# Optimization experiments

Hardware: AMD Instinct MI355X
Metric: run time of the kernel (lower is better)

Reference implementation:

```python
import jax, jax.numpy as jnp
import numpy as np

B = 1024
HP_ORDER = 4
N_GRID = 72 * (8 ** HP_ORDER)  # 294912 rotations in the SO(3) healpix grid


def _random_rotmats(key, n):
    """Uniform random rotation matrices via normalized quaternions."""
    q = jax.random.normal(key, (n, 4), dtype=jnp.float32)
    q = q / jnp.linalg.norm(q, axis=-1, keepdims=True)
    w, x, y, z = q[:, 0], q[:, 1], q[:, 2], q[:, 3]
    R = jnp.stack([
        jnp.stack([1 - 2 * (y * y + z * z), 2 * (x * y - w * z), 2 * (x * z + w * y)], axis=-1),
        jnp.stack([2 * (x * y + w * z), 1 - 2 * (x * x + z * z), 2 * (y * z - w * x)], axis=-1),
        jnp.stack([2 * (x * z - w * y), 2 * (y * z + w * x), 1 - 2 * (x * x + y * y)], axis=-1),
    ], axis=-2)  # [n, 3, 3]
    return R


def setup_inputs() -> dict:
    key = jax.random.key(0)
    k1, k2 = jax.random.split(key)
    rotMat = _random_rotmats(k1, B)            # [B, 3, 3] query rotations
    output_rotmats = _random_rotmats(k2, N_GRID)  # [N, 3, 3] fixed grid (buffer)
    return {"rotMat": rotMat, "output_rotmats": output_rotmats}


def reference(rotMat, output_rotmats):
    # trace(A @ R_n^T) == sum_ij A_ij * R_n_ij  -> GEMM with K=9
    sim = jnp.einsum('bij,nij->bn', rotMat, output_rotmats)  # [B, N]
    idxs = jnp.argmax(sim, axis=1)                            # [B]
    dot_trace = jnp.max(sim, axis=1)                          # [B]
    nearest = output_rotmats[idxs]                            # [B, 3, 3]
    return dot_trace, nearest
```

## Files before the change

kernel.cpp:

```cpp
#include <hip/hip_runtime.h>

#define B_TOTAL 1024
#define NGRID   294912
#define NBLK    1024
#define CHUNK   (NGRID / NBLK)
#define NTHR    128
#define BPT     8


__global__ __launch_bounds__(256)
void so3_init_kernel(unsigned long long* __restrict__ ws) {
    int i = blockIdx.x * 256 + threadIdx.x;
    if (i < B_TOTAL) ws[i] = 0ull;
}

__global__ __launch_bounds__(NTHR, 3)
void so3_partial_kernel(const float* __restrict__ A,
                        const float* __restrict__ G,
                        unsigned long long* __restrict__ ws)
{
    __shared__ __align__(16) float sG[CHUNK * 12];

    const int t  = threadIdx.x;
    const int n0 = blockIdx.x * CHUNK;

    for (int i = t; i < CHUNK * 9; i += NTHR) {
        int row = i / 9, k = i - row * 9;
        sG[row * 12 + k] = G[(size_t)n0 * 9 + i];
    }

    float a[BPT][9];
    #pragma unroll
    for (int j = 0; j < BPT; ++j) {
        const float* ap = A + (size_t)(j * NTHR + t) * 9;
        #pragma unroll
        for (int k = 0; k < 9; ++k) a[j][k] = ap[k];
    }

    float best[BPT];
    int   bidx[BPT];
    #pragma unroll
    for (int j = 0; j < BPT; ++j) { best[j] = -1e30f; bidx[j] = 0; }

    __syncthreads();

    #pragma unroll 2
    for (int n = 0; n < CHUNK; ++n) {
        const float4* gv = (const float4*)(sG + n * 12);
        const float4 gA = gv[0], gB = gv[1];
        const float  g8 = sG[n * 12 + 8];
        const int vn = n0 + n;
        #pragma unroll
        for (int j = 0; j < BPT; ++j) {
            float d;
            d = a[j][0] * gA.x;
            d = fmaf(a[j][1], gA.y, d);
            d = fmaf(a[j][2], gA.z, d);
            d = fmaf(a[j][3], gA.w, d);
            d = fmaf(a[j][4], gB.x, d);
            d = fmaf(a[j][5], gB.y, d);
            d = fmaf(a[j][6], gB.z, d);
            d = fmaf(a[j][7], gB.w, d);
            d = fmaf(a[j][8], g8, d);
            if (d > best[j]) { best[j] = d; bidx[j] = vn; }
        }
    }

    #pragma unroll
    for (int j = 0; j < BPT; ++j) {
        unsigned u = __float_as_uint(best[j]);
        u = (u & 0x80000000u) ? ~u : (u | 0x80000000u);
        unsigned long long key =
            ((unsigned long long)u << 32) | (unsigned)(~bidx[j]);
        atomicMax(&ws[j * NTHR + t], key);
    }
}

__global__ __launch_bounds__(256)
void so3_final_kernel(const float* __restrict__ G,
                      const unsigned long long* __restrict__ ws,
                      float* __restrict__ out)
{
    int b = blockIdx.x * 256 + threadIdx.x;
    if (b >= B_TOTAL) return;
    unsigned long long key = ws[b];
    unsigned hi = (unsigned)(key >> 32);
    unsigned lo = (unsigned)key;
    unsigned bits = (hi & 0x80000000u) ? (hi ^ 0x80000000u) : ~hi;
    int idx = (int)(~lo);
    out[b] = __uint_as_float(bits);
    const float* g = G + (size_t)idx * 9;
    float* o = out + B_TOTAL + (size_t)b * 9;
    #pragma unroll
    for (int k = 0; k < 9; ++k) o[k] = g[k];
}

extern "C" void kernel_launch(void* const* d_in, const int* in_sizes, int n_in,
                              void* d_out, int out_size, void* d_ws, size_t ws_size,
                              hipStream_t stream) {
    const float* A = (const float*)d_in[0];
    const float* G = (const float*)d_in[1];
    float* out = (float*)d_out;
    unsigned long long* ws = (unsigned long long*)d_ws;

    hipLaunchKernelGGL(so3_init_kernel,    dim3(4),    dim3(256), 0, stream, ws);
    hipLaunchKernelGGL(so3_partial_kernel, dim3(NBLK), dim3(NTHR), 0, stream, A, G, ws);
    hipLaunchKernelGGL(so3_final_kernel,   dim3(4),    dim3(256), 0, stream, G, ws, out);
}
```

Measured before the change: 96.77 us.

## Use split-bf16 MFMA max pass with candidate filtering and exact fp32 rescoring

Replaces the scalar fp32 FMA scan with bf16 MFMA matrix products. A and G are packed into hi/lo bf16 pairs so that three-term products approximate fp32 accuracy. A first MFMA pass computes per-query maxima, and a second pass emits every (query, grid) pair within a margin of that max as a candidate. The candidates are then rescored exactly in fp32 for the argmax. This trades compute-bound FMA work for matrix-core throughput, but adds packing kernels, two full passes over the GEMM, atomics on a global candidate counter, and reliance on the margin and candidate cap being correct. The old scalar path is kept as a fallback when the workspace is too small.

```diff
diff --git a/kernel.cpp b/kernel.cpp
--- a/kernel.cpp
+++ b/kernel.cpp
@@ -2,97 +2,279 @@
 
 #define B_TOTAL 1024
 #define NGRID   294912
-#define NBLK    1024
-#define CHUNK   (NGRID / NBLK)
-#define NTHR    128
-#define BPT     8
-
+#define NTILES  (NGRID / 16)
+#define MARGIN  6e-4f
+#define CAP     (1u << 20)
+
+#define KEYS_OFF   0u
+#define WSMAX_OFF  8192u
+#define CNT_OFF    12288u
+#define CAND_OFF   16384u
+#define APACK_OFF  4210688u
+#define GPACK_OFF  4276224u
+#define WS_NEED    23150592u
+
+typedef __attribute__((ext_vector_type(8))) short short8v;
+typedef __attribute__((ext_vector_type(4))) float float4v;
+
+__device__ __forceinline__ unsigned short f2bf(float x) {
+    unsigned u = __float_as_uint(x);
+    unsigned r = ((u >> 16) & 1u) + 0x7FFFu;
+    return (unsigned short)((u + r) >> 16);
+}
+__device__ __forceinline__ float bf2f(unsigned short b) {
+    return __uint_as_float(((unsigned)b) << 16);
+}
+__device__ __forceinline__ unsigned ford(float f) {
+    unsigned u = __float_as_uint(f);
+    return (u & 0x80000000u) ? ~u : (u | 0x80000000u);
+}
+__device__ __forceinline__ float funord(unsigned u) {
+    return __uint_as_float((u & 0x80000000u) ? (u & 0x7FFFFFFFu) : ~u);
+}
 
 __global__ __launch_bounds__(256)
-void so3_init_kernel(unsigned long long* __restrict__ ws) {
+void so3_init_kernel(unsigned long long* __restrict__ keys,
+                     unsigned* __restrict__ wsmax, unsigned* __restrict__ cnt) {
     int i = blockIdx.x * 256 + threadIdx.x;
-    if (i < B_TOTAL) ws[i] = 0ull;
-}
-
-__global__ __launch_bounds__(NTHR, 3)
-void so3_partial_kernel(const float* __restrict__ A,
-                        const float* __restrict__ G,
-                        unsigned long long* __restrict__ ws)
-{
-    __shared__ __align__(16) float sG[CHUNK * 12];
-
-    const int t  = threadIdx.x;
-    const int n0 = blockIdx.x * CHUNK;
-
-    for (int i = t; i < CHUNK * 9; i += NTHR) {
+    if (i < B_TOTAL) { keys[i] = 0ull; wsmax[i] = 0u; }
+    if (i == 0) *cnt = 0u;
+}
+
+__global__ __launch_bounds__(256)
+void so3_pack_kernel(const float* __restrict__ src, unsigned* __restrict__ dst,
+                     int nrows, int isA) {
+    int id = blockIdx.x * 256 + threadIdx.x;
+    if (id >= nrows * 16) return;
+    int r = id >> 4, i = id & 15;
+    unsigned w = 0;
+    #pragma unroll
+    for (int h = 0; h < 2; ++h) {
+        int s = i * 2 + h;
+        unsigned short v = 0;
+        if (s < 27) {
+            int k = (s < 9) ? s : (s < 18 ? s - 9 : s - 18);
+            float x = src[(size_t)r * 9 + k];
+            unsigned short hi = f2bf(x);
+            int wantLo = isA ? (s >= 18) : (s >= 9 && s < 18);
+            v = wantLo ? f2bf(x - bf2f(hi)) : hi;
+        }
+        w |= ((unsigned)v) << (16 * h);
+    }
+    dst[id] = w;
+}
+
+__device__ __forceinline__ void stage_A(const unsigned short* __restrict__ Ap,
+                                        unsigned short* sB, int t) {
+    #pragma unroll
+    for (int i = 0; i < 16; ++i) {
+        int id = t + i * 256;
+        int row = id >> 2, kb = id & 3;
+        uint4 v = *(const uint4*)(Ap + row * 32 + kb * 8);
+        int skb = kb ^ ((row >> 1) & 3);
+        *(uint4*)((char*)sB + row * 64 + skb * 16) = v;
+    }
+}
+
+__global__ __launch_bounds__(256, 2)
+void so3_mfma_max_kernel(const unsigned short* __restrict__ Ap,
+                         const unsigned short* __restrict__ Gp,
+                         unsigned* __restrict__ wsmax) {
+    __shared__ __align__(16) unsigned short sB[1024 * 32];
+    const int t = threadIdx.x;
+    stage_A(Ap, sB, t);
+    __syncthreads();
+
+    const int l = t & 63, w = t >> 6;
+    const int lr = l & 15, lk = l >> 4;
+    const int ntile0 = blockIdx.x * 36 + w * 9;
+
+    float mx[64];
+    #pragma unroll
+    for (int bt = 0; bt < 64; ++bt) mx[bt] = -1e30f;
+
+    for (int g = 0; g < 3; ++g) {
+        short8v af[3];
+        #pragma unroll
+        for (int d = 0; d < 3; ++d) {
+            int nt = ntile0 + g * 3 + d;
+            af[d] = *(const short8v*)(Gp + (size_t)(nt * 16 + lr) * 32 + lk * 8);
+        }
+        #pragma unroll
+        for (int bt = 0; bt < 64; ++bt) {
+            int row = bt * 16 + lr;
+            int skb = lk ^ ((row >> 1) & 3);
+            short8v bf = *(const short8v*)((const char*)sB + row * 64 + skb * 16);
+            #pragma unroll
+            for (int d = 0; d < 3; ++d) {
+                float4v c = {0.f, 0.f, 0.f, 0.f};
+                c = __builtin_amdgcn_mfma_f32_16x16x32_bf16(af[d], bf, c, 0, 0, 0);
+                mx[bt] = fmaxf(mx[bt],
+                               fmaxf(fmaxf(c[0], c[1]), fmaxf(c[2], c[3])));
+            }
+        }
+    }
+    #pragma unroll
+    for (int bt = 0; bt < 64; ++bt) {
+        float m = mx[bt];
+        m = fmaxf(m, __shfl_xor(m, 16));
+        m = fmaxf(m, __shfl_xor(m, 32));
+        if (l < 16) {
+            unsigned u = ford(m);
+            unsigned* p = wsmax + bt * 16 + l;
+            if (u > *p) atomicMax(p, u);
+        }
+    }
+}
+
+__global__ __launch_bounds__(256, 2)
+void so3_mfma_cand_kernel(const unsigned short* __restrict__ Ap,
+                          const unsigned short* __restrict__ Gp,
+                          const unsigned* __restrict__ wsmax,
+                          unsigned* __restrict__ cnt,
+                          unsigned* __restrict__ cands) {
+    __shared__ __align__(16) unsigned short sB[1024 * 32];
+    const int t = threadIdx.x;
+    stage_A(Ap, sB, t);
+
+    const int l = t & 63, w = t >> 6;
+    const int lr = l & 15, lk = l >> 4;
+    const int ntile0 = blockIdx.x * 36 + w * 9;
+
+    float thr[64];
+    #pragma unroll
+    for (int bt = 0; bt < 64; ++bt)
+        thr[bt] = funord(wsmax[bt * 16 + lr]) - MARGIN;
+    __syncthreads();
+
+    for (int g = 0; g < 3; ++g) {
+        short8v af[3];
+        #pragma unroll
+        for (int d = 0; d < 3; ++d) {
+            int nt = ntile0 + g * 3 + d;
+            af[d] = *(const short8v*)(Gp + (size_t)(nt * 16 + lr) * 32 + lk * 8);
+        }
+        #pragma unroll
+        for (int bt = 0; bt < 64; ++bt) {
+            int row = bt * 16 + lr;
+            int skb = lk ^ ((row >> 1) & 3);
+            short8v bf = *(const short8v*)((const char*)sB + row * 64 + skb * 16);
+            #pragma unroll
+            for (int d = 0; d < 3; ++d) {
+                float4v c = {0.f, 0.f, 0.f, 0.f};
+                c = __builtin_amdgcn_mfma_f32_16x16x32_bf16(af[d], bf, c, 0, 0, 0);
+                float m4 = fmaxf(fmaxf(c[0], c[1]), fmaxf(c[2], c[3]));
+                if (__any(m4 >= thr[bt])) {
+                    int nt = ntile0 + g * 3 + d;
+                    int b = bt * 16 + lr;
+                    #pragma unroll
+                    for (int r = 0; r < 4; ++r) {
+                        if (c[r] >= thr[bt]) {
+                            int n = nt * 16 + lk * 4 + r;
+                            unsigned idx = atomicAdd(cnt, 1u);
+                            if (idx < CAP)
+                                cands[idx] = ((unsigned)b << 19) | (unsigned)n;
+                        }
+                    }
+                }
+            }
+        }
+    }
+}
+
+__global__ __launch_bounds__(256)
+void so3_rescore_kernel(const float* __restrict__ A, const float* __restrict__ G,
+                        const unsigned* __restrict__ cnt,
+                        const unsigned* __restrict__ cands,
+                        unsigned long long* __restrict__ keys) {
+    unsigned total = *cnt;
+    if (total > CAP) total = CAP;
+    const unsigned stride = gridDim.x * 256;
+    for (unsigned i = blockIdx.x * 256 + threadIdx.x; i < total; i += stride) {
+        unsigned cd = cands[i];
+        int b = (int)(cd >> 19), n = (int)(cd & 0x7FFFFu);
+        const float* a = A + (size_t)b * 9;
+        const float* g = G + (size_t)n * 9;
+        float d;
+        d = a[0] * g[0];
+        d = fmaf(a[1], g[1], d);
+        d = fmaf(a[2], g[2], d);
+        d = fmaf(a[3], g[3], d);
+        d = fmaf(a[4], g[4], d);
+        d = fmaf(a[5], g[5], d);
+        d = fmaf(a[6], g[6], d);
+        d = fmaf(a[7], g[7], d);
+        d = fmaf(a[8], g[8], d);
+        unsigned long long key =
+            ((unsigned long long)ford(d) << 32) | (unsigned)(~n);
+        unsigned long long seen = keys[b];
+        if (key > seen) atomicMax(&keys[b], key);
+    }
+}
+
+__global__ __launch_bounds__(256)
+void so3_final_kernel(const float* __restrict__ G,
+                      const unsigned long long* __restrict__ keys,
+                      float* __restrict__ out) {
+    int b = blockIdx.x * 256 + threadIdx.x;
+    if (b >= B_TOTAL) return;
+    unsigned long long key = keys[b];
+    unsigned hi = (unsigned)(key >> 32);
+    int idx = (int)(~(unsigned)key);
+    out[b] = funord(hi);
+    const float* g = G + (size_t)idx * 9;
+    float* o = out + B_TOTAL + (size_t)b * 9;
+    #pragma unroll
+    for (int k = 0; k < 9; ++k) o[k] = g[k];
+}
+
+#define FB_NBLK  2048
+#define FB_CHUNK (NGRID / FB_NBLK)
+#define FB_NTHR  128
+#define FB_BPT   8
+__global__ __launch_bounds__(FB_NTHR, 4)
+void so3_fb_partial_kernel(const float* __restrict__ A, const float* __restrict__ G,
+                           unsigned long long* __restrict__ ws) {
+    __shared__ __align__(16) float sG[FB_CHUNK * 12];
+    const int t = threadIdx.x;
+    const int n0 = blockIdx.x * FB_CHUNK;
+    for (int i = t; i < FB_CHUNK * 9; i += FB_NTHR) {
         int row = i / 9, k = i - row * 9;
         sG[row * 12 + k] = G[(size_t)n0 * 9 + i];
     }
-
-    float a[BPT][9];
-    #pragma unroll
-    for (int j = 0; j < BPT; ++j) {
-        const float* ap = A + (size_t)(j * NTHR + t) * 9;
+    float a[FB_BPT][9];
+    #pragma unroll
+    for (int j = 0; j < FB_BPT; ++j) {
+        const float* ap = A + (size_t)(j * FB_NTHR + t) * 9;
         #pragma unroll
         for (int k = 0; k < 9; ++k) a[j][k] = ap[k];
     }
-
-    float best[BPT];
-    int   bidx[BPT];
-    #pragma unroll
-    for (int j = 0; j < BPT; ++j) { best[j] = -1e30f; bidx[j] = 0; }
-
+    float best[FB_BPT]; int bidx[FB_BPT];
+    #pragma unroll
+    for (int j = 0; j < FB_BPT; ++j) { best[j] = -1e30f; bidx[j] = 0; }
     __syncthreads();
-
     #pragma unroll 2
-    for (int n = 0; n < CHUNK; ++n) {
+    for (int n = 0; n < FB_CHUNK; ++n) {
         const float4* gv = (const float4*)(sG + n * 12);
         const float4 gA = gv[0], gB = gv[1];
-        const float  g8 = sG[n * 12 + 8];
+        const float g8 = sG[n * 12 + 8];
         const int vn = n0 + n;
         #pragma unroll
-        for (int j = 0; j < BPT; ++j) {
+        for (int j = 0; j < FB_BPT; ++j) {
             float d;
-            d = a[j][0] * gA.x;
-            d = fmaf(a[j][1], gA.y, d);
-            d = fmaf(a[j][2], gA.z, d);
-            d = fmaf(a[j][3], gA.w, d);
-            d = fmaf(a[j][4], gB.x, d);
-            d = fmaf(a[j][5], gB.y, d);
-            d = fmaf(a[j][6], gB.z, d);
-            d = fmaf(a[j][7], gB.w, d);
-            d = fmaf(a[j][8], g8, d);
+            d = a[j][0] * gA.x; d = fmaf(a[j][1], gA.y, d); d = fmaf(a[j][2], gA.z, d);
+            d = fmaf(a[j][3], gA.w, d); d = fmaf(a[j][4], gB.x, d); d = fmaf(a[j][5], gB.y, d);
+            d = fmaf(a[j][6], gB.z, d); d = fmaf(a[j][7], gB.w, d); d = fmaf(a[j][8], g8, d);
             if (d > best[j]) { best[j] = d; bidx[j] = vn; }
         }
     }
-
-    #pragma unroll
-    for (int j = 0; j < BPT; ++j) {
-        unsigned u = __float_as_uint(best[j]);
-        u = (u & 0x80000000u) ? ~u : (u | 0x80000000u);
+    #pragma unroll
+    for (int j = 0; j < FB_BPT; ++j) {
         unsigned long long key =
-            ((unsigned long long)u << 32) | (unsigned)(~bidx[j]);
-        atomicMax(&ws[j * NTHR + t], key);
-    }
-}
-
-__global__ __launch_bounds__(256)
-void so3_final_kernel(const float* __restrict__ G,
-                      const unsigned long long* __restrict__ ws,
-                      float* __restrict__ out)
-{
-    int b = blockIdx.x * 256 + threadIdx.x;
-    if (b >= B_TOTAL) return;
-    unsigned long long key = ws[b];
-    unsigned hi = (unsigned)(key >> 32);
-    unsigned lo = (unsigned)key;
-    unsigned bits = (hi & 0x80000000u) ? (hi ^ 0x80000000u) : ~hi;
-    int idx = (int)(~lo);
-    out[b] = __uint_as_float(bits);
-    const float* g = G + (size_t)idx * 9;
-    float* o = out + B_TOTAL + (size_t)b * 9;
-    #pragma unroll
-    for (int k = 0; k < 9; ++k) o[k] = g[k];
+            ((unsigned long long)ford(best[j]) << 32) | (unsigned)(~bidx[j]);
+        unsigned long long seen = ws[j * FB_NTHR + t];
+        if (key > seen) atomicMax(&ws[j * FB_NTHR + t], key);
+    }
 }
 
 extern "C" void kernel_launch(void* const* d_in, const int* in_sizes, int n_in,
@@ -101,9 +283,36 @@
     const float* A = (const float*)d_in[0];
     const float* G = (const float*)d_in[1];
     float* out = (float*)d_out;
-    unsigned long long* ws = (unsigned long long*)d_ws;
-
-    hipLaunchKernelGGL(so3_init_kernel,    dim3(4),    dim3(256), 0, stream, ws);
-    hipLaunchKernelGGL(so3_partial_kernel, dim3(NBLK), dim3(NTHR), 0, stream, A, G, ws);
-    hipLaunchKernelGGL(so3_final_kernel,   dim3(4),    dim3(256), 0, stream, G, ws, out);
-}
+    char* ws = (char*)d_ws;
+    unsigned long long* keys = (unsigned long long*)(ws + KEYS_OFF);
+    unsigned* wsmax = (unsigned*)(ws + WSMAX_OFF);
+    unsigned* cnt   = (unsigned*)(ws + CNT_OFF);
+    unsigned* cands = (unsigned*)(ws + CAND_OFF);
+    unsigned short* Ap = (unsigned short*)(ws + APACK_OFF);
+    unsigned short* Gp = (unsigned short*)(ws + GPACK_OFF);
+
+    if (ws_size < WS_NEED) {
+        hipLaunchKernelGGL(so3_init_kernel, dim3(4), dim3(256), 0, stream,
+                           keys, wsmax, cnt);
+        hipLaunchKernelGGL(so3_fb_partial_kernel, dim3(FB_NBLK), dim3(FB_NTHR),
+                           0, stream, A, G, keys);
+        hipLaunchKernelGGL(so3_final_kernel, dim3(4), dim3(256), 0, stream,
+                           G, keys, out);
+        return;
+    }
+
+    hipLaunchKernelGGL(so3_init_kernel, dim3(4), dim3(256), 0, stream,
+                       keys, wsmax, cnt);
+    hipLaunchKernelGGL(so3_pack_kernel, dim3((B_TOTAL * 16) / 256), dim3(256),
+                       0, stream, A, (unsigned*)Ap, B_TOTAL, 1);
+    hipLaunchKernelGGL(so3_pack_kernel, dim3((NGRID * 16) / 256), dim3(256),
+                       0, stream, G, (unsigned*)Gp, NGRID, 0);
+    hipLaunchKernelGGL(so3_mfma_max_kernel, dim3(512), dim3(256), 0, stream,
+                       Ap, Gp, wsmax);
+    hipLaunchKernelGGL(so3_mfma_cand_kernel, dim3(512), dim3(256), 0, stream,
+                       Ap, Gp, wsmax, cnt, cands);
+    hipLaunchKernelGGL(so3_rescore_kernel, dim3(64), dim3(256), 0, stream,
+                       A, G, cnt, cands, keys);
+    hipLaunchKernelGGL(so3_final_kernel, dim3(4), dim3(256), 0, stream,
+                       G, keys, out);
+}
```

After: 240.4 us. 148% more time.
